# Kernel tuning notes

Hardware: AMD Instinct MI355X
Metric: run time of the kernel (lower is better)

Reference implementation:

```python
import jax, jax.numpy as jnp
import numpy as np

D_MODEL = 1024
NUM_HEADS = 16
D_K = D_MODEL // NUM_HEADS


def setup_inputs() -> dict:
    key = jax.random.key(0)
    ks = jax.random.split(key, 11)
    B, S, D = 4, 2048, D_MODEL
    scale = 1.0 / np.sqrt(D)
    return {
        "Q": jax.random.normal(ks[0], (B, S, D), jnp.float32),
        "K": jax.random.normal(ks[1], (B, S, D), jnp.float32),
        "V": jax.random.normal(ks[2], (B, S, D), jnp.float32),
        "Wq": jax.random.normal(ks[3], (D, D), jnp.float32) * scale,
        "bq": jnp.zeros((D,), jnp.float32),
        "Wk": jax.random.normal(ks[4], (D, D), jnp.float32) * scale,
        "bk": jnp.zeros((D,), jnp.float32),
        "Wv": jax.random.normal(ks[5], (D, D), jnp.float32) * scale,
        "bv": jnp.zeros((D,), jnp.float32),
        "Wo": jax.random.normal(ks[6], (D, D), jnp.float32) * scale,
        "bo": jnp.zeros((D,), jnp.float32),
    }


def reference(Q, K, V, Wq, bq, Wk, bk, Wv, bv, Wo, bo):
    B, S, D = Q.shape
    H, Dk = NUM_HEADS, D_K
    # projections: [B,S,D] -> [B,H,S,Dk]
    def proj(x, W, b):
        y = jnp.einsum('bsd,de->bse', x, W.T) + b  # torch Linear: x @ W.T + b
        return y.reshape(B, -1, H, Dk).transpose(0, 2, 1, 3)
    q = proj(Q, Wq, bq)
    k = proj(K, Wk, bk)
    v = proj(V, Wv, bv)
    scores = jnp.einsum('bhqd,bhkd->bhqk', q, k) / np.sqrt(Dk)  # [B,H,S,S]
    attn = jax.nn.softmax(scores, axis=-1)
    out = jnp.einsum('bhqk,bhkd->bhqd', attn, v)  # [B,H,S,Dk]
    out = out.transpose(0, 2, 1, 3).reshape(B, -1, D)
    return jnp.einsum('bsd,de->bse', out, Wo.T) + bo
```

## Files before the change

kernel.cpp:

```cpp
#include <hip/hip_runtime.h>


typedef __bf16 bhalf_t;
typedef __attribute__((ext_vector_type(8)))  __bf16 bf16x8;
typedef __attribute__((ext_vector_type(4)))  __bf16 bf16x4;
typedef __attribute__((ext_vector_type(4)))  float  f32x4;
typedef __attribute__((ext_vector_type(16))) float  f32x16;

typedef __attribute__((address_space(1))) void gvoid_t;
typedef __attribute__((address_space(3))) void lvoid_t;
#define GLD16(g, l) __builtin_amdgcn_global_load_lds((const gvoid_t*)(g), (lvoid_t*)(l), 16, 0, 0)

__global__ __launch_bounds__(256) void cvt_all(
    const float* __restrict__ Q, const float* __restrict__ Kin, const float* __restrict__ V,
    const float* __restrict__ Wq, const float* __restrict__ Wk, const float* __restrict__ Wv,
    const float* __restrict__ Wo,
    bhalf_t* __restrict__ Qb, bhalf_t* __restrict__ Kb, bhalf_t* __restrict__ Vb,
    bhalf_t* __restrict__ Wqb, bhalf_t* __restrict__ Wkb, bhalf_t* __restrict__ Wvb,
    bhalf_t* __restrict__ Wob)
{
  size_t t = (size_t)blockIdx.x * 256 + threadIdx.x;
  const float* src; bhalf_t* dst;
  if (t < 2097152)      { src = Q;   dst = Qb; }
  else if (t < 4194304) { src = Kin; dst = Kb; t -= 2097152; }
  else if (t < 6291456) { src = V;   dst = Vb; t -= 4194304; }
  else {
    t -= 6291456;
    int w = (int)(t >> 18); t &= 262143;
    src = (w == 0) ? Wq  : (w == 1) ? Wk  : (w == 2) ? Wv  : Wo;
    dst = (w == 0) ? Wqb : (w == 1) ? Wkb : (w == 2) ? Wvb : Wob;
  }
  float4 f = ((const float4*)src)[t];
  bf16x4 o;
  o.x = (bhalf_t)f.x; o.y = (bhalf_t)f.y; o.z = (bhalf_t)f.z; o.w = (bhalf_t)f.w;
  ((bf16x4*)dst)[t] = o;
}

__device__ __forceinline__ void gemm_core_128(
    const bhalf_t* __restrict__ A, const bhalf_t* __restrict__ B,
    int bm, int bn, bhalf_t* As, bhalf_t* Bs, f32x4 acc[4][4])
{
  const int tid = threadIdx.x, lane = tid & 63, wave = tid >> 6;
  const int wm = wave >> 1, wn = wave & 1;
  const int quad = lane >> 4, tn = lane & 15;
  const int srow = lane >> 2, scol = (lane & 3) * 8;

  const bhalf_t* Ab0 = A + (size_t)(bm * 128 + wave * 16 + srow) * 1024 + scol;
  const bhalf_t* Ab1 = Ab0 + (size_t)64 * 1024;
  const bhalf_t* Bb0 = B + (size_t)(bn * 128 + wave * 16 + srow) * 1024 + scol;
  const bhalf_t* Bb1 = Bb0 + (size_t)64 * 1024;
  bhalf_t* Asw0 = As + wave * 512;  bhalf_t* Asw1 = As + (wave + 4) * 512;
  bhalf_t* Bsw0 = Bs + wave * 512;  bhalf_t* Bsw1 = Bs + (wave + 4) * 512;

  for (int k0 = 0; k0 < 1024; k0 += 32) {
    GLD16(Ab0 + k0, Asw0);
    GLD16(Ab1 + k0, Asw1);
    GLD16(Bb0 + k0, Bsw0);
    GLD16(Bb1 + k0, Bsw1);
    __syncthreads();
    bf16x8 af[4], bfr[4];
#pragma unroll
    for (int i = 0; i < 4; ++i)
      af[i] = *(const bf16x8*)(As + (wm * 64 + i * 16 + tn) * 32 + quad * 8);
#pragma unroll
    for (int j = 0; j < 4; ++j)
      bfr[j] = *(const bf16x8*)(Bs + (wn * 64 + j * 16 + tn) * 32 + quad * 8);
#pragma unroll
    for (int i = 0; i < 4; ++i)
#pragma unroll
      for (int j = 0; j < 4; ++j)
        acc[i][j] = __builtin_amdgcn_mfma_f32_16x16x32_bf16(af[i], bfr[j], acc[i][j], 0, 0, 0);
    __syncthreads();
  }
}

__global__ __launch_bounds__(256) void proj_gemm(
    const bhalf_t* __restrict__ Qb, const bhalf_t* __restrict__ Kb, const bhalf_t* __restrict__ Vb,
    const bhalf_t* __restrict__ Wqb, const bhalf_t* __restrict__ Wkb, const bhalf_t* __restrict__ Wvb,
    const float* __restrict__ bq, const float* __restrict__ bk, const float* __restrict__ bv,
    bhalf_t* __restrict__ qo, bhalf_t* __restrict__ ko, bhalf_t* __restrict__ vto)
{
  __shared__ bhalf_t As[4096];
  __shared__ bhalf_t Bs[4096];
  const int seg = blockIdx.x >> 9;
  const int idx = blockIdx.x & 511;
  const int bm = idx >> 3, bn = idx & 7;

  const bhalf_t *A, *Bw; const float* bias; bhalf_t* out; float scale; int mode;
  if (seg == 0)      { A = Qb; Bw = Wqb; bias = bq; out = qo;  scale = 0.125f; mode = 0; }
  else if (seg == 1) { A = Kb; Bw = Wkb; bias = bk; out = ko;  scale = 1.0f;   mode = 0; }
  else               { A = Vb; Bw = Wvb; bias = bv; out = vto; scale = 1.0f;   mode = 1; }

  f32x4 acc[4][4];
#pragma unroll
  for (int i = 0; i < 4; ++i)
#pragma unroll
    for (int j = 0; j < 4; ++j)
      acc[i][j] = (f32x4){0.f, 0.f, 0.f, 0.f};

  gemm_core_128(A, Bw, bm, bn, As, Bs, acc);

  const int lane = threadIdx.x & 63, wave = threadIdx.x >> 6;
  const int wm = wave >> 1, wn = wave & 1, quad = lane >> 4, tn = lane & 15;
#pragma unroll
  for (int i = 0; i < 4; ++i)
#pragma unroll
    for (int j = 0; j < 4; ++j) {
      const int n = bn * 128 + wn * 64 + j * 16 + tn;
      const float bsv = bias[n];
      const int h = n >> 6, dk = n & 63;
#pragma unroll
      for (int r = 0; r < 4; ++r) {
        const int m = bm * 128 + wm * 64 + i * 16 + quad * 4 + r;
        const int b = m >> 11, s = m & 2047;
        const float v = (acc[i][j][r] + bsv) * scale;
        size_t addr;
        if (mode == 0) addr = (((size_t)(b * 16 + h)) * 2048 + s) * 64 + dk;
        else           addr = (((size_t)(b * 16 + h)) * 64 + dk) * 2048 + s;
        out[addr] = (bhalf_t)v;
      }
    }
}

__global__ __launch_bounds__(256) void out_gemm(
    const bhalf_t* __restrict__ A, const bhalf_t* __restrict__ Bw,
    const float* __restrict__ bias, float* __restrict__ Cout)
{
  __shared__ bhalf_t As[4096];
  __shared__ bhalf_t Bs[4096];
  const int bm = blockIdx.x >> 3, bn = blockIdx.x & 7;

  f32x4 acc[4][4];
#pragma unroll
  for (int i = 0; i < 4; ++i)
#pragma unroll
    for (int j = 0; j < 4; ++j)
      acc[i][j] = (f32x4){0.f, 0.f, 0.f, 0.f};

  gemm_core_128(A, Bw, bm, bn, As, Bs, acc);

  const int lane = threadIdx.x & 63, wave = threadIdx.x >> 6;
  const int wm = wave >> 1, wn = wave & 1, quad = lane >> 4, tn = lane & 15;
#pragma unroll
  for (int i = 0; i < 4; ++i)
#pragma unroll
    for (int j = 0; j < 4; ++j) {
      const int n = bn * 128 + wn * 64 + j * 16 + tn;
      const float bsv = bias[n];
#pragma unroll
      for (int r = 0; r < 4; ++r) {
        const int m = bm * 128 + wm * 64 + i * 16 + quad * 4 + r;
        Cout[(size_t)m * 1024 + n] = acc[i][j][r] + bsv;
      }
    }
}

__global__ __launch_bounds__(256, 4) void attn_kernel(
    const bhalf_t* __restrict__ qp, const bhalf_t* __restrict__ kp,
    const bhalf_t* __restrict__ vtp, bhalf_t* __restrict__ outp)
{
  __shared__ bhalf_t Klds[4096];
  __shared__ bhalf_t Vtlds[4096];
  __shared__ bhalf_t Plds[4 * 32 * 72];

  const int tid = threadIdx.x, lane = tid & 63, wave = tid >> 6;
  const int q31 = lane & 31, h = lane >> 5;
  const int bh = blockIdx.y, qt = blockIdx.x;

  const bhalf_t* qbase = qp + (((size_t)bh * 2048) + qt * 128 + wave * 32 + q31) * 64;
  bf16x8 qf[4];
#pragma unroll
  for (int ks = 0; ks < 4; ++ks)
    qf[ks] = *(const bf16x8*)(qbase + ks * 16 + h * 8);

  f32x16 Ot[2];
#pragma unroll
  for (int mb = 0; mb < 2; ++mb)
#pragma unroll
    for (int i = 0; i < 16; ++i) Ot[mb][i] = 0.f;
  float Lp = 0.f;

  const bhalf_t* kbase  = kp  + (size_t)bh * 2048 * 64;
  const bhalf_t* vtbase = vtp + (size_t)bh * 64 * 2048;
  bhalf_t* Pw = Plds + wave * 2304;

  const int rloc = lane >> 3;
  const int cg8  = ((lane & 7) ^ rloc) * 8;
  const int asw0 = ((0 + h) ^ (q31 & 7)) * 8;
  const int asw1 = ((2 + h) ^ (q31 & 7)) * 8;
  const int asw2 = ((4 + h) ^ (q31 & 7)) * 8;
  const int asw3 = ((6 + h) ^ (q31 & 7)) * 8;
  const int aswz[4] = {asw0, asw1, asw2, asw3};

  for (int kv0 = 0; kv0 < 2048; kv0 += 64) {
#pragma unroll
    for (int i = 0; i < 2; ++i) {
      const int r0 = (wave * 2 + i) * 8;
      GLD16(kbase + (size_t)(kv0 + r0 + rloc) * 64 + cg8, Klds + r0 * 64);
      GLD16(vtbase + (size_t)(r0 + rloc) * 2048 + kv0 + cg8, Vtlds + r0 * 64);
    }
    __syncthreads();

#pragma unroll
    for (int mb = 0; mb < 2; ++mb) {
      f32x16 S;
#pragma unroll
      for (int i = 0; i < 16; ++i) S[i] = 0.f;
      const int rbase = mb * 32 + q31;
#pragma unroll
      for (int ks = 0; ks < 4; ++ks) {
        const bf16x8 ka = *(const bf16x8*)(Klds + rbase * 64 + ks * 16 + (aswz[ks] - ks * 16));
        S = __builtin_amdgcn_mfma_f32_32x32x16_bf16(ka, qf[ks], S, 0, 0, 0);
      }
#pragma unroll
      for (int g = 0; g < 4; ++g) {
        const float e0 = __expf(S[4 * g + 0]);
        const float e1 = __expf(S[4 * g + 1]);
        const float e2 = __expf(S[4 * g + 2]);
        const float e3 = __expf(S[4 * g + 3]);
        Lp += (e0 + e1) + (e2 + e3);
        bf16x4 pk;
        pk.x = (bhalf_t)e0; pk.y = (bhalf_t)e1; pk.z = (bhalf_t)e2; pk.w = (bhalf_t)e3;
        *(bf16x4*)(Pw + q31 * 72 + mb * 32 + g * 8 + h * 4) = pk;
      }
    }

#pragma unroll
    for (int ks = 0; ks < 4; ++ks) {
      const bf16x8 pb = *(const bf16x8*)(Pw + q31 * 72 + ks * 16 + h * 8);
#pragma unroll
      for (int mb = 0; mb < 2; ++mb) {
        const bf16x8 va = *(const bf16x8*)(Vtlds + (mb * 32 + q31) * 64 + aswz[ks]);
        Ot[mb] = __builtin_amdgcn_mfma_f32_32x32x16_bf16(va, pb, Ot[mb], 0, 0, 0);
      }
    }
    __syncthreads();
  }

  const float Lt = Lp + __shfl_xor(Lp, 32, 64);
  const float linv = 1.0f / Lt;
  const int b = bh >> 4, hh = bh & 15;
  const int s = qt * 128 + wave * 32 + q31;
  bhalf_t* ob = outp + ((size_t)(b * 2048 + s)) * 1024 + hh * 64;
#pragma unroll
  for (int mb = 0; mb < 2; ++mb)
#pragma unroll
    for (int g = 0; g < 4; ++g) {
      bf16x4 o;
      o.x = (bhalf_t)(Ot[mb][4 * g + 0] * linv);
      o.y = (bhalf_t)(Ot[mb][4 * g + 1] * linv);
      o.z = (bhalf_t)(Ot[mb][4 * g + 2] * linv);
      o.w = (bhalf_t)(Ot[mb][4 * g + 3] * linv);
      *(bf16x4*)(ob + mb * 32 + g * 8 + h * 4) = o;
    }
}

extern "C" void kernel_launch(void* const* d_in, const int* in_sizes, int n_in,
                              void* d_out, int out_size, void* d_ws, size_t ws_size,
                              hipStream_t stream)
{
  const float* Q  = (const float*)d_in[0];
  const float* K  = (const float*)d_in[1];
  const float* V  = (const float*)d_in[2];
  const float* Wq = (const float*)d_in[3];
  const float* bq = (const float*)d_in[4];
  const float* Wk = (const float*)d_in[5];
  const float* bk = (const float*)d_in[6];
  const float* Wv = (const float*)d_in[7];
  const float* bv = (const float*)d_in[8];
  const float* Wo = (const float*)d_in[9];
  const float* bo = (const float*)d_in[10];

  char* ws = (char*)d_ws;
  const size_t SZ = 8192ull * 1024 * 2;
  const size_t WZ = 1024ull * 1024 * 2;
  bhalf_t* Qb   = (bhalf_t*)(ws);
  bhalf_t* Kb   = (bhalf_t*)(ws + SZ);
  bhalf_t* Vb   = (bhalf_t*)(ws + 2 * SZ);
  bhalf_t* Wqb  = (bhalf_t*)(ws + 3 * SZ);
  bhalf_t* Wkb  = (bhalf_t*)(ws + 3 * SZ + WZ);
  bhalf_t* Wvb  = (bhalf_t*)(ws + 3 * SZ + 2 * WZ);
  bhalf_t* Wob  = (bhalf_t*)(ws + 3 * SZ + 3 * WZ);
  bhalf_t* q_p  = (bhalf_t*)(ws + 3 * SZ + 4 * WZ);
  bhalf_t* k_p  = (bhalf_t*)(ws + 4 * SZ + 4 * WZ);
  bhalf_t* vt_p = (bhalf_t*)(ws + 5 * SZ + 4 * WZ);
  bhalf_t* attn_o = Qb;

  cvt_all<<<28672, 256, 0, stream>>>(Q, K, V, Wq, Wk, Wv, Wo,
                                     Qb, Kb, Vb, Wqb, Wkb, Wvb, Wob);
  proj_gemm<<<1536, 256, 0, stream>>>(Qb, Kb, Vb, Wqb, Wkb, Wvb,
                                      bq, bk, bv, q_p, k_p, vt_p);
  attn_kernel<<<dim3(16, 64), 256, 0, stream>>>(q_p, k_p, vt_p, attn_o);
  out_gemm<<<512, 256, 0, stream>>>(attn_o, Wob, bo, (float*)d_out);
}
```

Before: 373.1 us.

## Keep P in registers via permuted V layout and double queries per wave

Drops the LDS round-trip for the softmax probabilities. V is stored with a permuted sequence order so the MFMA output fragment of S can be fed straight back as the B operand of the PV MFMA. Each wave now handles 64 queries instead of 32, reusing K/V LDS fragments across two query sub-tiles, and the block tile grows to 256 queries. The Q scale folds in log2(e) so exp2 replaces expf. The cost is higher register pressure, lowered occupancy bounds (2 blocks) and half as many blocks in the grid.

```diff
diff --git a/kernel.cpp b/kernel.cpp
--- a/kernel.cpp
+++ b/kernel.cpp
@@ -87,9 +87,9 @@
   const int bm = idx >> 3, bn = idx & 7;
 
   const bhalf_t *A, *Bw; const float* bias; bhalf_t* out; float scale; int mode;
-  if (seg == 0)      { A = Qb; Bw = Wqb; bias = bq; out = qo;  scale = 0.125f; mode = 0; }
-  else if (seg == 1) { A = Kb; Bw = Wkb; bias = bk; out = ko;  scale = 1.0f;   mode = 0; }
-  else               { A = Vb; Bw = Wvb; bias = bv; out = vto; scale = 1.0f;   mode = 1; }
+  if (seg == 0)      { A = Qb; Bw = Wqb; bias = bq; out = qo;  scale = 0.18033688f; mode = 0; }
+  else if (seg == 1) { A = Kb; Bw = Wkb; bias = bk; out = ko;  scale = 1.0f;        mode = 0; }
+  else               { A = Vb; Bw = Wvb; bias = bv; out = vto; scale = 1.0f;        mode = 1; }
 
   f32x4 acc[4][4];
 #pragma unroll
@@ -116,7 +116,10 @@
         const float v = (acc[i][j][r] + bsv) * scale;
         size_t addr;
         if (mode == 0) addr = (((size_t)(b * 16 + h)) * 2048 + s) * 64 + dk;
-        else           addr = (((size_t)(b * 16 + h)) * 64 + dk) * 2048 + s;
+        else {
+          const int s2 = (s & ~12) | ((s & 4) << 1) | ((s & 8) >> 1);
+          addr = (((size_t)(b * 16 + h)) * 64 + dk) * 2048 + s2;
+        }
         out[addr] = (bhalf_t)v;
       }
     }
@@ -155,42 +158,40 @@
     }
 }
 
-__global__ __launch_bounds__(256, 4) void attn_kernel(
+__global__ __launch_bounds__(256, 2) void attn_kernel(
     const bhalf_t* __restrict__ qp, const bhalf_t* __restrict__ kp,
     const bhalf_t* __restrict__ vtp, bhalf_t* __restrict__ outp)
 {
   __shared__ bhalf_t Klds[4096];
   __shared__ bhalf_t Vtlds[4096];
-  __shared__ bhalf_t Plds[4 * 32 * 72];
 
   const int tid = threadIdx.x, lane = tid & 63, wave = tid >> 6;
   const int q31 = lane & 31, h = lane >> 5;
   const int bh = blockIdx.y, qt = blockIdx.x;
 
-  const bhalf_t* qbase = qp + (((size_t)bh * 2048) + qt * 128 + wave * 32 + q31) * 64;
-  bf16x8 qf[4];
-#pragma unroll
-  for (int ks = 0; ks < 4; ++ks)
-    qf[ks] = *(const bf16x8*)(qbase + ks * 16 + h * 8);
-
-  f32x16 Ot[2];
-#pragma unroll
-  for (int mb = 0; mb < 2; ++mb)
-#pragma unroll
-    for (int i = 0; i < 16; ++i) Ot[mb][i] = 0.f;
-  float Lp = 0.f;
+  const bhalf_t* qbase = qp + (((size_t)bh * 2048) + qt * 256 + wave * 64 + q31) * 64;
+  bf16x8 qf[2][4];
+#pragma unroll
+  for (int qs = 0; qs < 2; ++qs)
+#pragma unroll
+    for (int ks = 0; ks < 4; ++ks)
+      qf[qs][ks] = *(const bf16x8*)(qbase + qs * 32 * 64 + ks * 16 + h * 8);
+
+  f32x16 Ot[2][2];
+#pragma unroll
+  for (int qs = 0; qs < 2; ++qs)
+#pragma unroll
+    for (int dd = 0; dd < 2; ++dd)
+#pragma unroll
+      for (int i = 0; i < 16; ++i) Ot[qs][dd][i] = 0.f;
+  float Lp[2] = {0.f, 0.f};
 
   const bhalf_t* kbase  = kp  + (size_t)bh * 2048 * 64;
   const bhalf_t* vtbase = vtp + (size_t)bh * 64 * 2048;
-  bhalf_t* Pw = Plds + wave * 2304;
 
   const int rloc = lane >> 3;
   const int cg8  = ((lane & 7) ^ rloc) * 8;
-  const int asw0 = ((0 + h) ^ (q31 & 7)) * 8;
-  const int asw1 = ((2 + h) ^ (q31 & 7)) * 8;
-  const int asw2 = ((4 + h) ^ (q31 & 7)) * 8;
-  const int asw3 = ((6 + h) ^ (q31 & 7)) * 8;
-  const int aswz[4] = {asw0, asw1, asw2, asw3};
+  const int q7 = q31 & 7;
 
   for (int kv0 = 0; kv0 < 2048; kv0 += 64) {
 #pragma unroll
@@ -201,58 +202,68 @@
     }
     __syncthreads();
 
+    bf16x8 pb[2][4];
 #pragma unroll
     for (int mb = 0; mb < 2; ++mb) {
-      f32x16 S;
-#pragma unroll
-      for (int i = 0; i < 16; ++i) S[i] = 0.f;
-      const int rbase = mb * 32 + q31;
-#pragma unroll
-      for (int ks = 0; ks < 4; ++ks) {
-        const bf16x8 ka = *(const bf16x8*)(Klds + rbase * 64 + ks * 16 + (aswz[ks] - ks * 16));
-        S = __builtin_amdgcn_mfma_f32_32x32x16_bf16(ka, qf[ks], S, 0, 0, 0);
-      }
-#pragma unroll
-      for (int g = 0; g < 4; ++g) {
-        const float e0 = __expf(S[4 * g + 0]);
-        const float e1 = __expf(S[4 * g + 1]);
-        const float e2 = __expf(S[4 * g + 2]);
-        const float e3 = __expf(S[4 * g + 3]);
-        Lp += (e0 + e1) + (e2 + e3);
-        bf16x4 pk;
-        pk.x = (bhalf_t)e0; pk.y = (bhalf_t)e1; pk.z = (bhalf_t)e2; pk.w = (bhalf_t)e3;
-        *(bf16x4*)(Pw + q31 * 72 + mb * 32 + g * 8 + h * 4) = pk;
+      bf16x8 ka[4];
+#pragma unroll
+      for (int ks = 0; ks < 4; ++ks)
+        ka[ks] = *(const bf16x8*)(Klds + (mb * 32 + q31) * 64 + ((2 * ks + h) ^ q7) * 8);
+#pragma unroll
+      for (int qs = 0; qs < 2; ++qs) {
+        f32x16 S;
+#pragma unroll
+        for (int i = 0; i < 16; ++i) S[i] = 0.f;
+#pragma unroll
+        for (int ks = 0; ks < 4; ++ks)
+          S = __builtin_amdgcn_mfma_f32_32x32x16_bf16(ka[ks], qf[qs][ks], S, 0, 0, 0);
+        float ls = 0.f;
+#pragma unroll
+        for (int half = 0; half < 2; ++half) {
+          bf16x8 pk;
+#pragma unroll
+          for (int j = 0; j < 8; ++j) {
+            const float e = __builtin_amdgcn_exp2f(S[half * 8 + j]);
+            ls += e;
+            pk[j] = (bhalf_t)e;
+          }
+          pb[qs][mb * 2 + half] = pk;
+        }
+        Lp[qs] += ls;
       }
     }
 
 #pragma unroll
-    for (int ks = 0; ks < 4; ++ks) {
-      const bf16x8 pb = *(const bf16x8*)(Pw + q31 * 72 + ks * 16 + h * 8);
-#pragma unroll
-      for (int mb = 0; mb < 2; ++mb) {
-        const bf16x8 va = *(const bf16x8*)(Vtlds + (mb * 32 + q31) * 64 + aswz[ks]);
-        Ot[mb] = __builtin_amdgcn_mfma_f32_32x32x16_bf16(va, pb, Ot[mb], 0, 0, 0);
-      }
-    }
+    for (int dd = 0; dd < 2; ++dd)
+#pragma unroll
+      for (int kb = 0; kb < 4; ++kb) {
+        const bf16x8 va = *(const bf16x8*)(Vtlds + (dd * 32 + q31) * 64 + ((2 * kb + h) ^ q7) * 8);
+#pragma unroll
+        for (int qs = 0; qs < 2; ++qs)
+          Ot[qs][dd] = __builtin_amdgcn_mfma_f32_32x32x16_bf16(va, pb[qs][kb], Ot[qs][dd], 0, 0, 0);
+      }
     __syncthreads();
   }
 
-  const float Lt = Lp + __shfl_xor(Lp, 32, 64);
-  const float linv = 1.0f / Lt;
   const int b = bh >> 4, hh = bh & 15;
-  const int s = qt * 128 + wave * 32 + q31;
-  bhalf_t* ob = outp + ((size_t)(b * 2048 + s)) * 1024 + hh * 64;
-#pragma unroll
-  for (int mb = 0; mb < 2; ++mb)
-#pragma unroll
-    for (int g = 0; g < 4; ++g) {
-      bf16x4 o;
-      o.x = (bhalf_t)(Ot[mb][4 * g + 0] * linv);
-      o.y = (bhalf_t)(Ot[mb][4 * g + 1] * linv);
-      o.z = (bhalf_t)(Ot[mb][4 * g + 2] * linv);
-      o.w = (bhalf_t)(Ot[mb][4 * g + 3] * linv);
-      *(bf16x4*)(ob + mb * 32 + g * 8 + h * 4) = o;
-    }
+#pragma unroll
+  for (int qs = 0; qs < 2; ++qs) {
+    const float Lt = Lp[qs] + __shfl_xor(Lp[qs], 32, 64);
+    const float linv = 1.0f / Lt;
+    const int s = qt * 256 + wave * 64 + qs * 32 + q31;
+    bhalf_t* ob = outp + ((size_t)(b * 2048 + s)) * 1024 + hh * 64;
+#pragma unroll
+    for (int dd = 0; dd < 2; ++dd)
+#pragma unroll
+      for (int g = 0; g < 4; ++g) {
+        bf16x4 o;
+        o.x = (bhalf_t)(Ot[qs][dd][4 * g + 0] * linv);
+        o.y = (bhalf_t)(Ot[qs][dd][4 * g + 1] * linv);
+        o.z = (bhalf_t)(Ot[qs][dd][4 * g + 2] * linv);
+        o.w = (bhalf_t)(Ot[qs][dd][4 * g + 3] * linv);
+        *(bf16x4*)(ob + dd * 32 + g * 8 + h * 4) = o;
+      }
+  }
 }
 
 extern "C" void kernel_launch(void* const* d_in, const int* in_sizes, int n_in,
@@ -290,6 +301,6 @@
                                      Qb, Kb, Vb, Wqb, Wkb, Wvb, Wob);
   proj_gemm<<<1536, 256, 0, stream>>>(Qb, Kb, Vb, Wqb, Wkb, Wvb,
                                       bq, bk, bv, q_p, k_p, vt_p);
-  attn_kernel<<<dim3(16, 64), 256, 0, stream>>>(q_p, k_p, vt_p, attn_o);
+  attn_kernel<<<dim3(8, 64), 256, 0, stream>>>(q_p, k_p, vt_p, attn_o);
   out_gemm<<<512, 256, 0, stream>>>(attn_o, Wob, bo, (float*)d_out);
 }
```

After: 348.8 us. 6.5% less time.
